# Optimization experiments

Hardware: AMD Instinct MI355X
Metric: run time of the kernel (lower is better)

Reference implementation:

```python
import jax, jax.numpy as jnp
import numpy as np

B, T, D, F = 32, 512, 512, 256
K = 3
MEL_MAX = 4096
EPS = 1e-5


def _xavier(key, shape, fan_in, fan_out):
    lim = float(np.sqrt(6.0 / (fan_in + fan_out)))
    return jax.random.uniform(key, shape, jnp.float32, -lim, lim)


def setup_inputs() -> dict:
    key = jax.random.key(0)
    ks = jax.random.split(key, 6)
    x = jax.random.normal(ks[0], (B, T, D), jnp.float32)
    target = jax.random.randint(ks[1], (B, T), 0, 8)  # per-token durations
    # conv weights stored as [K, I, O] (lax 'WIO'); torch xavier on [O,I,K]: fan_in=I*K, fan_out=O*K
    w1 = _xavier(ks[2], (K, D, F), D * K, F * K)
    b1 = jnp.zeros((F,), jnp.float32)
    g1 = jnp.ones((F,), jnp.float32)
    be1 = jnp.zeros((F,), jnp.float32)
    w2 = _xavier(ks[3], (K, F, F), F * K, F * K)
    b2 = jnp.zeros((F,), jnp.float32)
    g2 = jnp.ones((F,), jnp.float32)
    be2 = jnp.zeros((F,), jnp.float32)
    wl = _xavier(ks[4], (F, 1), F, 1)
    bl = jnp.zeros((1,), jnp.float32)
    return dict(x=x, target=target, mel_max_length=MEL_MAX,
                w1=w1, b1=b1, g1=g1, be1=be1,
                w2=w2, b2=b2, g2=g2, be2=be2, wl=wl, bl=bl)


def _layer_norm(h, g, b):
    mu = jnp.mean(h, axis=-1, keepdims=True)
    var = jnp.mean(jnp.square(h - mu), axis=-1, keepdims=True)
    return (h - mu) * jax.lax.rsqrt(var + EPS) * g + b


def _conv1d(h, w, b):
    # h: [B,T,C_in], w: [K,C_in,C_out]; torch padding=1 with K=3 == SAME
    out = jax.lax.conv_general_dilated(h, w, (1,), 'SAME',
                                       dimension_numbers=('NWC', 'WIO', 'NWC'))
    return out + b


def reference(x, target, mel_max_length, w1, b1, g1, be1, w2, b2, g2, be2, wl, bl):
    # ---- DurationPredictor (eval: dropout = identity) ----
    h = jax.nn.relu(_layer_norm(_conv1d(x, w1, b1), g1, be1))
    h = jax.nn.relu(_layer_norm(_conv1d(h, w2, b2), g2, be2))
    dur_pred = jax.nn.relu(h @ wl + bl)[..., 0]  # [B, T]

    # ---- LR: ragged expansion of x by `target` durations, padded to mel_max_length ----
    cum = jnp.cumsum(target, axis=1)              # [B, T]
    total = cum[:, -1]                            # [B]
    pos = jnp.arange(mel_max_length)              # [M]
    # frame m maps to token i with cum[i-1] <= m < cum[i]
    idx = jax.vmap(lambda c: jnp.searchsorted(c, pos, side='right'))(cum)  # [B, M]
    idx = jnp.clip(idx, 0, x.shape[1] - 1)
    mask = pos[None, :] < total[:, None]          # [B, M]
    out = jnp.take_along_axis(x, idx[..., None], axis=1) * mask[..., None].astype(x.dtype)
    return (out, dur_pred)
```

## Files before the change

### kernel.cpp

```cpp
#include <hip/hip_runtime.h>
#include <type_traits>

#define B_   32
#define T_   512
#define D_   512
#define F_   256
#define MEL  4096
#define EPS_ 1e-5f

typedef __attribute__((ext_vector_type(8))) short bf16x8;
typedef __attribute__((ext_vector_type(4))) float f32x4;

#define GLL16(gp, lp) \
    __builtin_amdgcn_global_load_lds((const __attribute__((address_space(1))) void*)(gp), \
                                     (__attribute__((address_space(3))) void*)(lp), 16, 0, 0)
#define BARRIER() do { asm volatile("" ::: "memory"); __builtin_amdgcn_s_barrier(); \
                       asm volatile("" ::: "memory"); } while (0)
#define MEMPIN() asm volatile("" ::: "memory")

__device__ inline unsigned short f2bf(float f) {
    unsigned u = __float_as_uint(f);
    unsigned r = (u + 0x7fff + ((u >> 16) & 1)) >> 16;
    return (unsigned short)r;
}

#define PREP_WBLOCKS 2304

__global__ __launch_bounds__(256)
void prep_kernel(const float* __restrict__ w1, const float* __restrict__ w2,
                 const int* __restrict__ tgt,
                 unsigned short* __restrict__ w1T, unsigned short* __restrict__ w2T,
                 int* __restrict__ gidx)
{
    __shared__ int lcum[T_];
    __shared__ int wsum[4];

    int bid = blockIdx.x;
    int tid = threadIdx.x;
    if (bid < PREP_WBLOCKS) {
        int idx = bid * 256 + tid;
        if (idx < 3 * D_ * F_) {
            int kk = idx / F_, f = idx % F_;
            w1T[(size_t)f * (3 * D_) + kk] = f2bf(w1[idx]);
        } else {
            int j = idx - 3 * D_ * F_;
            int kk = j / F_, f = j % F_;
            w2T[(size_t)f * (3 * F_) + kk] = f2bf(w2[j]);
        }
        return;
    }

    int b = bid - PREP_WBLOCKS;
    int t0 = tid * 2;
    int a0 = tgt[b * T_ + t0], a1 = tgt[b * T_ + t0 + 1];
    int lane = tid & 63, w = tid >> 6;
    int v = a0 + a1;
#pragma unroll
    for (int o = 1; o < 64; o <<= 1) { int u = __shfl_up(v, o); if (lane >= o) v += u; }
    if (lane == 63) wsum[w] = v;
    __syncthreads();
    int base = 0;
#pragma unroll
    for (int i = 0; i < 4; ++i) if (i < w) base += wsum[i];
    int incl = base + v;
    lcum[t0]     = incl - a1;
    lcum[t0 + 1] = incl;
    __syncthreads();

    int total = lcum[T_ - 1];
#pragma unroll
    for (int k = 0; k < MEL / 256; ++k) {
        int pos = tid + k * 256;
        int lo = 0, hi = T_;
        while (lo < hi) { int mid = (lo + hi) >> 1; if (lcum[mid] <= pos) lo = mid + 1; else hi = mid; }
        gidx[b * MEL + pos] = (pos < total) ? min(lo, T_ - 1) : -1;
    }
}

template<int IN_D, typename InT, bool FUSE_DUR, int GP, int GBASE>
__global__ __launch_bounds__(512)
void conv_mfma_kernel(const InT* __restrict__ x, const unsigned short* __restrict__ wT,
                      const float* __restrict__ bias, const float* __restrict__ gamma,
                      const float* __restrict__ beta, unsigned short* __restrict__ out,
                      const float* __restrict__ wl, const float* __restrict__ bl,
                      float* __restrict__ dur,
                      const float* __restrict__ xf, const int* __restrict__ gidx,
                      float* __restrict__ gout)
{
    constexpr int MT = 64;
    constexpr int KT = 3 * IN_D;
    constexpr int PHASES = KT / 64;

    __shared__ __align__(16) char xs_raw[(MT + 2) * IN_D * 2];
    __shared__ __align__(16) unsigned short xsB[2 * 16384];
    __shared__ float red[MT][8];
    __shared__ float redD[MT][4];

    const int blocksPerBatch = T_ / MT;
    const int b  = blockIdx.x / blocksPerBatch;
    const int t0 = (blockIdx.x % blocksPerBatch) * MT;
    const int l  = threadIdx.x & 63;
    const int wv = threadIdx.x >> 6;
    const int fg = wv & 3;
    const int rg = wv >> 2;

    constexpr int CH = (MT + 2) * IN_D / 8;
    for (int c = threadIdx.x; c < CH; c += 512) {
        int j  = c / (IN_D / 8);
        int d8 = (c % (IN_D / 8)) * 8;
        int t  = t0 - 1 + j;
        uint4 pk = make_uint4(0u, 0u, 0u, 0u);
        if (t >= 0 && t < T_) {
            if constexpr (std::is_same_v<InT, float>) {
                const float4* src = reinterpret_cast<const float4*>(&x[((size_t)b * T_ + t) * IN_D + d8]);
                float4 a0 = src[0], a1 = src[1];
                pk.x = (unsigned)f2bf(a0.x) | ((unsigned)f2bf(a0.y) << 16);
                pk.y = (unsigned)f2bf(a0.z) | ((unsigned)f2bf(a0.w) << 16);
                pk.z = (unsigned)f2bf(a1.x) | ((unsigned)f2bf(a1.y) << 16);
                pk.w = (unsigned)f2bf(a1.z) | ((unsigned)f2bf(a1.w) << 16);
            } else {
                pk = *reinterpret_cast<const uint4*>(&x[((size_t)b * T_ + t) * IN_D + d8]);
            }
        }
        int byte = ((j * IN_D + d8) * 2) ^ ((j & 7) << 4);
        *reinterpret_cast<uint4*>(&xs_raw[byte]) = pk;
    }

    float bv[4], gv[4], bev[4], wlv[4];
#pragma unroll
    for (int n = 0; n < 4; ++n) {
        int f = fg * 64 + n * 16 + (l & 15);
        bv[n] = bias[f]; gv[n] = gamma[f]; bev[n] = beta[f];
        if constexpr (FUSE_DUR) wlv[n] = wl[f];
    }
    float blv = 0.f;
    if constexpr (FUSE_DUR) blv = bl[0];

    asm volatile("s_waitcnt vmcnt(0)" ::: "memory");
    __syncthreads();

    constexpr int GROWS = 2 * GP;
    const int rbase = GBASE + (blockIdx.x * 8 + wv) * GROWS;
    int gidxv = gidx[rbase + min(l, GROWS - 1)];
    MEMPIN();

    const int sbase = wv * 4;
    auto stageB = [&](int ph, int buf) {
        int p = ph < PHASES ? ph : PHASES - 1;
        unsigned short* lb = &xsB[buf * 16384];
#pragma unroll
        for (int i = 0; i < 4; ++i) {
            int s = sbase + i;
            int c = s * 64 + l;
            int f = c >> 3;
            int kg = (c & 7) ^ (f & 7);
            const unsigned short* src = wT + (size_t)f * KT + p * 64 + kg * 8;
            GLL16(src, lb + s * 512);
        }
    };
    auto loadBfrag = [&](bf16x8* dst, int buf, int kk2) {
#pragma unroll
        for (int n = 0; n < 4; ++n) {
            int f  = fg * 64 + n * 16 + (l & 15);
            int kg = kk2 * 4 + (l >> 4);
            dst[n] = *reinterpret_cast<const bf16x8*>(&xsB[buf * 16384 + f * 64 + ((kg ^ (f & 7)) * 8)]);
        }
    };
    const int k_lane = (l >> 4) * 8;
    auto loadA = [&](bf16x8* dst, int kk) {
        int kp = kk / IN_D;
        int dbase = (kk % IN_D) + k_lane;
#pragma unroll
        for (int m = 0; m < 2; ++m) {
            int j = rg * 32 + m * 16 + (l & 15) + kp;
            int byte = ((j * IN_D + dbase) * 2) ^ ((j & 7) << 4);
            dst[m] = *reinterpret_cast<const bf16x8*>(&xs_raw[byte]);
        }
    };

    float4 ga[3][2][2];
    auto loadSet = [&](int slot, int s) {
#pragma unroll
        for (int i = 0; i < 2; ++i) {
            int li = 2 * s + i;
            int ix = __shfl(gidxv, li);
            int r  = rbase + li;
            const float* src = xf + ((size_t)(r >> 12) * T_ + max(ix, 0)) * D_ + l * 4;
            ga[slot][i][0] = *reinterpret_cast<const float4*>(src);
            ga[slot][i][1] = *reinterpret_cast<const float4*>(src + 256);
        }
    };
    auto storeSet = [&](int slot, int s) {
#pragma unroll
        for (int i = 0; i < 2; ++i) {
            int li = 2 * s + i;
            int ix = __shfl(gidxv, li);
            int r  = rbase + li;
            float4 a = ga[slot][i][0], c = ga[slot][i][1];
            if (ix < 0) { a = make_float4(0.f,0.f,0.f,0.f); c = make_float4(0.f,0.f,0.f,0.f); }
            float* d = gout + (size_t)r * D_ + l * 4;
            *reinterpret_cast<float4*>(d)       = a;
            *reinterpret_cast<float4*>(d + 256) = c;
        }
    };

    f32x4 acc[2][4];
#pragma unroll
    for (int m = 0; m < 2; ++m)
#pragma unroll
        for (int n = 0; n < 4; ++n) acc[m][n] = (f32x4){0.f, 0.f, 0.f, 0.f};

    stageB(0, 0);  MEMPIN();
    stageB(1, 1);  MEMPIN();
    loadSet(0, 0); MEMPIN();
    loadSet(1, 1); MEMPIN();

#pragma unroll
    for (int p = 0; p < PHASES; ++p) {
        const int nw = (p == 0) ? 12 : (p == 1) ? 16
                     : 4 * (1 + ((p >= 3 && p - 3 < GP) ? 1 : 0) + ((p < GP) ? 1 : 0) +
                                ((p - 2 < GP) ? 1 : 0) + ((p + 1 < GP) ? 1 : 0));
        if      (nw == 20) asm volatile("s_waitcnt vmcnt(20)" ::: "memory");
        else if (nw == 16) asm volatile("s_waitcnt vmcnt(16)" ::: "memory");
        else if (nw == 12) asm volatile("s_waitcnt vmcnt(12)" ::: "memory");
        else if (nw == 8)  asm volatile("s_waitcnt vmcnt(8)"  ::: "memory");
        else               asm volatile("s_waitcnt vmcnt(4)"  ::: "memory");
        BARRIER();
        int buf = p & 1;
#pragma unroll
        for (int kk2 = 0; kk2 < 2; ++kk2) {
            int kk = p * 64 + kk2 * 32;
            bf16x8 Bv[4], Av[2];
            loadBfrag(Bv, buf, kk2);
            loadA(Av, kk);
#pragma unroll
            for (int m = 0; m < 2; ++m)
#pragma unroll
                for (int n = 0; n < 4; ++n)
                    acc[m][n] = __builtin_amdgcn_mfma_f32_16x16x32_bf16(Av[m], Bv[n], acc[m][n], 0, 0, 0);
        }
        BARRIER();
        stageB(p + 2, buf);                                  MEMPIN();
        if (p >= 1 && p - 1 < GP) { storeSet((p - 1) % 3, p - 1); MEMPIN(); }
        if (p + 2 < GP)           { loadSet((p + 2) % 3, p + 2); MEMPIN(); }
    }
    if constexpr (GP >= PHASES) {
        storeSet((GP - 1) % 3, GP - 1);
    }

#pragma unroll
    for (int m = 0; m < 2; ++m)
#pragma unroll
        for (int q = 0; q < 4; ++q) {
            float s = 0.f, s2 = 0.f;
#pragma unroll
            for (int n = 0; n < 4; ++n) {
                float v2 = acc[m][n][q] + bv[n];
                acc[m][n][q] = v2;
                s += v2; s2 += v2 * v2;
            }
#pragma unroll
            for (int o = 1; o < 16; o <<= 1) { s += __shfl_xor(s, o); s2 += __shfl_xor(s2, o); }
            int row = rg * 32 + m * 16 + (l >> 4) * 4 + q;
            if ((l & 15) == 0) { red[row][fg * 2] = s; red[row][fg * 2 + 1] = s2; }
        }
    __syncthreads();

#pragma unroll
    for (int m = 0; m < 2; ++m)
#pragma unroll
        for (int q = 0; q < 4; ++q) {
            int row = rg * 32 + m * 16 + (l >> 4) * 4 + q;
            float s  = red[row][0] + red[row][2] + red[row][4] + red[row][6];
            float s2 = red[row][1] + red[row][3] + red[row][5] + red[row][7];
            float mu  = s * (1.f / F_);
            float var = s2 * (1.f / F_) - mu * mu;
            float rs  = rsqrtf(var + EPS_);
            size_t rb2 = ((size_t)(b * T_ + t0 + row)) * F_;
            float part = 0.f;
#pragma unroll
            for (int n = 0; n < 4; ++n) {
                float y = (acc[m][n][q] - mu) * rs * gv[n] + bev[n];
                y = fmaxf(y, 0.f);
                out[rb2 + fg * 64 + n * 16 + (l & 15)] = f2bf(y);
                if constexpr (FUSE_DUR) part = fmaf(y, wlv[n], part);
            }
            if constexpr (FUSE_DUR) {
#pragma unroll
                for (int o = 1; o < 16; o <<= 1) part += __shfl_xor(part, o);
                if ((l & 15) == 0) redD[row][fg] = part;
            }
        }

    if constexpr (FUSE_DUR) {
        __syncthreads();
        if (threadIdx.x < MT) {
            float s = redD[threadIdx.x][0] + redD[threadIdx.x][1]
                    + redD[threadIdx.x][2] + redD[threadIdx.x][3] + blv;
            dur[(size_t)b * T_ + t0 + threadIdx.x] = fmaxf(s, 0.f);
        }
    }
}

extern "C" void kernel_launch(void* const* d_in, const int* in_sizes, int n_in,
                              void* d_out, int out_size, void* d_ws, size_t ws_size,
                              hipStream_t stream)
{
    const float* x      = (const float*)d_in[0];
    const int*   target = (const int*)d_in[1];
    const float* w1  = (const float*)d_in[3];
    const float* b1  = (const float*)d_in[4];
    const float* g1  = (const float*)d_in[5];
    const float* be1 = (const float*)d_in[6];
    const float* w2  = (const float*)d_in[7];
    const float* b2  = (const float*)d_in[8];
    const float* g2  = (const float*)d_in[9];
    const float* be2 = (const float*)d_in[10];
    const float* wl  = (const float*)d_in[11];
    const float* bl  = (const float*)d_in[12];

    float* out = (float*)d_out;
    float* dur = out + (size_t)B_ * MEL * D_;

    char* ws = (char*)d_ws;
    unsigned short* w1T = (unsigned short*)ws;         ws += (size_t)F_ * (3 * D_) * 2;
    unsigned short* w2T = (unsigned short*)ws;         ws += (size_t)F_ * (3 * F_) * 2;
    unsigned short* h1  = (unsigned short*)ws;         ws += (size_t)B_ * T_ * F_ * 2;
    unsigned short* h2  = (unsigned short*)ws;         ws += (size_t)B_ * T_ * F_ * 2;
    int*            gidx = (int*)ws;

    prep_kernel<<<PREP_WBLOCKS + B_, 256, 0, stream>>>(w1, w2, target, w1T, w2T, gidx);

    conv_mfma_kernel<D_, float, false, 24, 0><<<B_ * (T_ / 64), 512, 0, stream>>>(
        x, w1T, b1, g1, be1, h1, nullptr, nullptr, nullptr, x, gidx, out);
    conv_mfma_kernel<F_, unsigned short, true, 8, 98304><<<B_ * (T_ / 64), 512, 0, stream>>>(
        h1, w2T, b2, g2, be2, h2, wl, bl, dur, x, gidx, out);
}
```

Measured before the change: 97.43 us.

## Load conv weight fragments directly from global into registers, drop LDS staging

Replaces the double-buffered LDS staging of weight tiles (global_load_lds plus barriers and hand-tuned vmcnt waits) with per-lane direct global loads of B fragments into a three-deep register ring, removing the per-phase block barriers. The interleaved gather load/store schedule is re-timed to the new 32-wide k-steps, and launch bounds request two blocks per CU since the LDS footprint shrinks. In exchange it adds register pressure, gives up LDS reuse of weights across waves (each wave fetches its own slices from L2), and issues uncoalesced strided global reads.

```diff
diff --git a/kernel.cpp b/kernel.cpp
--- a/kernel.cpp
+++ b/kernel.cpp
@@ -11,11 +11,6 @@
 typedef __attribute__((ext_vector_type(8))) short bf16x8;
 typedef __attribute__((ext_vector_type(4))) float f32x4;
 
-#define GLL16(gp, lp) \
-    __builtin_amdgcn_global_load_lds((const __attribute__((address_space(1))) void*)(gp), \
-                                     (__attribute__((address_space(3))) void*)(lp), 16, 0, 0)
-#define BARRIER() do { asm volatile("" ::: "memory"); __builtin_amdgcn_s_barrier(); \
-                       asm volatile("" ::: "memory"); } while (0)
 #define MEMPIN() asm volatile("" ::: "memory")
 
 __device__ inline unsigned short f2bf(float f) {
@@ -78,7 +73,7 @@
 }
 
 template<int IN_D, typename InT, bool FUSE_DUR, int GP, int GBASE>
-__global__ __launch_bounds__(512)
+__global__ __launch_bounds__(512, 2)
 void conv_mfma_kernel(const InT* __restrict__ x, const unsigned short* __restrict__ wT,
                       const float* __restrict__ bias, const float* __restrict__ gamma,
                       const float* __restrict__ beta, unsigned short* __restrict__ out,
@@ -89,10 +84,10 @@
 {
     constexpr int MT = 64;
     constexpr int KT = 3 * IN_D;
-    constexpr int PHASES = KT / 64;
+    constexpr int KSTEPS = KT / 32;
+    static_assert(2 * GP <= KSTEPS, "gather sets must fit in even steps");
 
     __shared__ __align__(16) char xs_raw[(MT + 2) * IN_D * 2];
-    __shared__ __align__(16) unsigned short xsB[2 * 16384];
     __shared__ float red[MT][8];
     __shared__ float redD[MT][4];
 
@@ -136,7 +131,6 @@
     float blv = 0.f;
     if constexpr (FUSE_DUR) blv = bl[0];
 
-    asm volatile("s_waitcnt vmcnt(0)" ::: "memory");
     __syncthreads();
 
     constexpr int GROWS = 2 * GP;
@@ -144,29 +138,16 @@
     int gidxv = gidx[rbase + min(l, GROWS - 1)];
     MEMPIN();
 
-    const int sbase = wv * 4;
-    auto stageB = [&](int ph, int buf) {
-        int p = ph < PHASES ? ph : PHASES - 1;
-        unsigned short* lb = &xsB[buf * 16384];
-#pragma unroll
-        for (int i = 0; i < 4; ++i) {
-            int s = sbase + i;
-            int c = s * 64 + l;
-            int f = c >> 3;
-            int kg = (c & 7) ^ (f & 7);
-            const unsigned short* src = wT + (size_t)f * KT + p * 64 + kg * 8;
-            GLL16(src, lb + s * 512);
+    const int f_lane = fg * 64 + (l & 15);
+    const int k_lane = (l >> 4) * 8;
+    auto loadB = [&](bf16x8* dst, int s) {
+        if (s < KSTEPS) {
+            const unsigned short* p = &wT[(size_t)f_lane * KT + s * 32 + k_lane];
+#pragma unroll
+            for (int n = 0; n < 4; ++n)
+                dst[n] = *reinterpret_cast<const bf16x8*>(p + (size_t)n * 16 * KT);
         }
     };
-    auto loadBfrag = [&](bf16x8* dst, int buf, int kk2) {
-#pragma unroll
-        for (int n = 0; n < 4; ++n) {
-            int f  = fg * 64 + n * 16 + (l & 15);
-            int kg = kk2 * 4 + (l >> 4);
-            dst[n] = *reinterpret_cast<const bf16x8*>(&xsB[buf * 16384 + f * 64 + ((kg ^ (f & 7)) * 8)]);
-        }
-    };
-    const int k_lane = (l >> 4) * 8;
     auto loadA = [&](bf16x8* dst, int kk) {
         int kp = kk / IN_D;
         int dbase = (kk % IN_D) + k_lane;
@@ -210,43 +191,35 @@
 #pragma unroll
         for (int n = 0; n < 4; ++n) acc[m][n] = (f32x4){0.f, 0.f, 0.f, 0.f};
 
-    stageB(0, 0);  MEMPIN();
-    stageB(1, 1);  MEMPIN();
-    loadSet(0, 0); MEMPIN();
-    loadSet(1, 1); MEMPIN();
-
-#pragma unroll
-    for (int p = 0; p < PHASES; ++p) {
-        const int nw = (p == 0) ? 12 : (p == 1) ? 16
-                     : 4 * (1 + ((p >= 3 && p - 3 < GP) ? 1 : 0) + ((p < GP) ? 1 : 0) +
-                                ((p - 2 < GP) ? 1 : 0) + ((p + 1 < GP) ? 1 : 0));
-        if      (nw == 20) asm volatile("s_waitcnt vmcnt(20)" ::: "memory");
-        else if (nw == 16) asm volatile("s_waitcnt vmcnt(16)" ::: "memory");
-        else if (nw == 12) asm volatile("s_waitcnt vmcnt(12)" ::: "memory");
-        else if (nw == 8)  asm volatile("s_waitcnt vmcnt(8)"  ::: "memory");
-        else               asm volatile("s_waitcnt vmcnt(4)"  ::: "memory");
-        BARRIER();
-        int buf = p & 1;
-#pragma unroll
-        for (int kk2 = 0; kk2 < 2; ++kk2) {
-            int kk = p * 64 + kk2 * 32;
-            bf16x8 Bv[4], Av[2];
-            loadBfrag(Bv, buf, kk2);
-            loadA(Av, kk);
+    bf16x8 Bq[3][4];
+    loadB(Bq[0], 0); MEMPIN();
+    loadB(Bq[1], 1); MEMPIN();
+    loadB(Bq[2], 2); MEMPIN();
+
+#pragma unroll
+    for (int s = 0; s < KSTEPS; ++s) {
+        bf16x8 Av[2];
+        loadA(Av, s * 32);
+        {
+            bf16x8* Bv = Bq[s % 3];
 #pragma unroll
             for (int m = 0; m < 2; ++m)
 #pragma unroll
                 for (int n = 0; n < 4; ++n)
                     acc[m][n] = __builtin_amdgcn_mfma_f32_16x16x32_bf16(Av[m], Bv[n], acc[m][n], 0, 0, 0);
         }
-        BARRIER();
-        stageB(p + 2, buf);                                  MEMPIN();
-        if (p >= 1 && p - 1 < GP) { storeSet((p - 1) % 3, p - 1); MEMPIN(); }
-        if (p + 2 < GP)           { loadSet((p + 2) % 3, p + 2); MEMPIN(); }
-    }
-    if constexpr (GP >= PHASES) {
-        storeSet((GP - 1) % 3, GP - 1);
-    }
+        MEMPIN();
+        loadB(Bq[s % 3], s + 3);
+        MEMPIN();
+        if ((s & 1) == 0) {
+            int q = s >> 1;
+            if (q >= 3 && q - 3 < GP) { storeSet((q - 3) % 3, q - 3); MEMPIN(); }
+            if (q < GP)               { loadSet(q % 3, q);            MEMPIN(); }
+        }
+    }
+#pragma unroll
+    for (int j = (KSTEPS / 2 >= 3 ? KSTEPS / 2 - 3 : 0); j < GP; ++j)
+        storeSet(j % 3, j);
 
 #pragma unroll
     for (int m = 0; m < 2; ++m)
```

Result: slower. 129.0 us (+32.4%).

## Fuse both conv layers into one kernel with halo recompute in LDS

Applied to the files above, without the earlier changes.

Merges the two conv+LayerNorm kernels into a single kernel. Each block computes conv1 for 66 rows (its 64 plus a one-row halo on each side), writes the activated result as bf16 into shared memory, then runs conv2 from LDS. This removes the h1/h2 global round trips and one launch. The gather of 64 output rows per wave is now spread over one kernel instead of two. The cost is redundant halo MFMA work done by a subset of waves, a larger LDS footprint that may limit occupancy, and the h2 global write is dropped since it was unused.

```diff
diff --git a/kernel.cpp b/kernel.cpp
--- a/kernel.cpp
+++ b/kernel.cpp
@@ -1,5 +1,4 @@
 #include <hip/hip_runtime.h>
-#include <type_traits>
 
 #define B_   32
 #define T_   512
@@ -7,6 +6,11 @@
 #define F_   256
 #define MEL  4096
 #define EPS_ 1e-5f
+
+#define PH1  24
+#define PH2  12
+#define PHT  36
+#define GP   32
 
 typedef __attribute__((ext_vector_type(8))) short bf16x8;
 typedef __attribute__((ext_vector_type(4))) float f32x4;
@@ -77,84 +81,75 @@
     }
 }
 
-template<int IN_D, typename InT, bool FUSE_DUR, int GP, int GBASE>
 __global__ __launch_bounds__(512)
-void conv_mfma_kernel(const InT* __restrict__ x, const unsigned short* __restrict__ wT,
-                      const float* __restrict__ bias, const float* __restrict__ gamma,
-                      const float* __restrict__ beta, unsigned short* __restrict__ out,
-                      const float* __restrict__ wl, const float* __restrict__ bl,
-                      float* __restrict__ dur,
-                      const float* __restrict__ xf, const int* __restrict__ gidx,
-                      float* __restrict__ gout)
+void fused_kernel(const float* __restrict__ x,
+                  const unsigned short* __restrict__ w1T, const unsigned short* __restrict__ w2T,
+                  const float* __restrict__ b1, const float* __restrict__ g1, const float* __restrict__ be1,
+                  const float* __restrict__ b2, const float* __restrict__ g2, const float* __restrict__ be2,
+                  const float* __restrict__ wl, const float* __restrict__ bl,
+                  const int* __restrict__ gidx,
+                  float* __restrict__ out, float* __restrict__ dur)
 {
-    constexpr int MT = 64;
-    constexpr int KT = 3 * IN_D;
-    constexpr int PHASES = KT / 64;
-
-    __shared__ __align__(16) char xs_raw[(MT + 2) * IN_D * 2];
+    __shared__ __align__(16) char xsA[84 * 512 * 2];
     __shared__ __align__(16) unsigned short xsB[2 * 16384];
-    __shared__ float red[MT][8];
-    __shared__ float redD[MT][4];
-
-    const int blocksPerBatch = T_ / MT;
-    const int b  = blockIdx.x / blocksPerBatch;
-    const int t0 = (blockIdx.x % blocksPerBatch) * MT;
+    __shared__ float red[80][8];
+    __shared__ float redD[64][4];
+
+    const int b  = blockIdx.x >> 3;
+    const int t0 = (blockIdx.x & 7) * 64;
     const int l  = threadIdx.x & 63;
     const int wv = threadIdx.x >> 6;
     const int fg = wv & 3;
     const int rg = wv >> 2;
 
-    constexpr int CH = (MT + 2) * IN_D / 8;
-    for (int c = threadIdx.x; c < CH; c += 512) {
-        int j  = c / (IN_D / 8);
-        int d8 = (c % (IN_D / 8)) * 8;
-        int t  = t0 - 1 + j;
+    for (int c = threadIdx.x; c < 68 * 64; c += 512) {
+        int j  = c >> 6;
+        int d8 = (c & 63) * 8;
+        int t  = t0 - 2 + j;
         uint4 pk = make_uint4(0u, 0u, 0u, 0u);
         if (t >= 0 && t < T_) {
-            if constexpr (std::is_same_v<InT, float>) {
-                const float4* src = reinterpret_cast<const float4*>(&x[((size_t)b * T_ + t) * IN_D + d8]);
-                float4 a0 = src[0], a1 = src[1];
-                pk.x = (unsigned)f2bf(a0.x) | ((unsigned)f2bf(a0.y) << 16);
-                pk.y = (unsigned)f2bf(a0.z) | ((unsigned)f2bf(a0.w) << 16);
-                pk.z = (unsigned)f2bf(a1.x) | ((unsigned)f2bf(a1.y) << 16);
-                pk.w = (unsigned)f2bf(a1.z) | ((unsigned)f2bf(a1.w) << 16);
-            } else {
-                pk = *reinterpret_cast<const uint4*>(&x[((size_t)b * T_ + t) * IN_D + d8]);
-            }
-        }
-        int byte = ((j * IN_D + d8) * 2) ^ ((j & 7) << 4);
-        *reinterpret_cast<uint4*>(&xs_raw[byte]) = pk;
-    }
-
-    float bv[4], gv[4], bev[4], wlv[4];
+            const float4* src = reinterpret_cast<const float4*>(&x[((size_t)b * T_ + t) * D_ + d8]);
+            float4 a0 = src[0], a1 = src[1];
+            pk.x = (unsigned)f2bf(a0.x) | ((unsigned)f2bf(a0.y) << 16);
+            pk.y = (unsigned)f2bf(a0.z) | ((unsigned)f2bf(a0.w) << 16);
+            pk.z = (unsigned)f2bf(a1.x) | ((unsigned)f2bf(a1.y) << 16);
+            pk.w = (unsigned)f2bf(a1.z) | ((unsigned)f2bf(a1.w) << 16);
+        }
+        int byte = ((j * 512 + d8) * 2) ^ ((j & 7) << 4);
+        *reinterpret_cast<uint4*>(&xsA[byte]) = pk;
+    }
+
+    float bv1[4], gv1[4], bev1[4], bv2[4], gv2[4], bev2[4], wlv[4];
 #pragma unroll
     for (int n = 0; n < 4; ++n) {
         int f = fg * 64 + n * 16 + (l & 15);
-        bv[n] = bias[f]; gv[n] = gamma[f]; bev[n] = beta[f];
-        if constexpr (FUSE_DUR) wlv[n] = wl[f];
-    }
-    float blv = 0.f;
-    if constexpr (FUSE_DUR) blv = bl[0];
+        bv1[n] = b1[f]; gv1[n] = g1[f]; bev1[n] = be1[f];
+        bv2[n] = b2[f]; gv2[n] = g2[f]; bev2[n] = be2[f];
+        wlv[n] = wl[f];
+    }
+    float blv = bl[0];
 
     asm volatile("s_waitcnt vmcnt(0)" ::: "memory");
     __syncthreads();
 
-    constexpr int GROWS = 2 * GP;
-    const int rbase = GBASE + (blockIdx.x * 8 + wv) * GROWS;
-    int gidxv = gidx[rbase + min(l, GROWS - 1)];
+    const int rbase = (blockIdx.x * 8 + wv) * 64;
+    int gidxv = gidx[rbase + l];
     MEMPIN();
 
     const int sbase = wv * 4;
     auto stageB = [&](int ph, int buf) {
-        int p = ph < PHASES ? ph : PHASES - 1;
         unsigned short* lb = &xsB[buf * 16384];
+        const unsigned short* wsrc;
+        int KTc, phc;
+        if (ph < PH1) { wsrc = w1T; KTc = 1536; phc = ph; }
+        else          { wsrc = w2T; KTc = 768;  phc = (ph - PH1 < PH2) ? ph - PH1 : PH2 - 1; }
 #pragma unroll
         for (int i = 0; i < 4; ++i) {
             int s = sbase + i;
             int c = s * 64 + l;
             int f = c >> 3;
             int kg = (c & 7) ^ (f & 7);
-            const unsigned short* src = wT + (size_t)f * KT + p * 64 + kg * 8;
+            const unsigned short* src = wsrc + (size_t)f * KTc + phc * 64 + kg * 8;
             GLL16(src, lb + s * 512);
         }
     };
@@ -167,16 +162,6 @@
         }
     };
     const int k_lane = (l >> 4) * 8;
-    auto loadA = [&](bf16x8* dst, int kk) {
-        int kp = kk / IN_D;
-        int dbase = (kk % IN_D) + k_lane;
-#pragma unroll
-        for (int m = 0; m < 2; ++m) {
-            int j = rg * 32 + m * 16 + (l & 15) + kp;
-            int byte = ((j * IN_D + dbase) * 2) ^ ((j & 7) << 4);
-            dst[m] = *reinterpret_cast<const bf16x8*>(&xs_raw[byte]);
-        }
-    };
 
     float4 ga[3][2][2];
     auto loadSet = [&](int slot, int s) {
@@ -185,7 +170,7 @@
             int li = 2 * s + i;
             int ix = __shfl(gidxv, li);
             int r  = rbase + li;
-            const float* src = xf + ((size_t)(r >> 12) * T_ + max(ix, 0)) * D_ + l * 4;
+            const float* src = x + ((size_t)(r >> 12) * T_ + max(ix, 0)) * D_ + l * 4;
             ga[slot][i][0] = *reinterpret_cast<const float4*>(src);
             ga[slot][i][1] = *reinterpret_cast<const float4*>(src + 256);
         }
@@ -198,17 +183,20 @@
             int r  = rbase + li;
             float4 a = ga[slot][i][0], c = ga[slot][i][1];
             if (ix < 0) { a = make_float4(0.f,0.f,0.f,0.f); c = make_float4(0.f,0.f,0.f,0.f); }
-            float* d = gout + (size_t)r * D_ + l * 4;
+            float* d = out + (size_t)r * D_ + l * 4;
             *reinterpret_cast<float4*>(d)       = a;
             *reinterpret_cast<float4*>(d + 256) = c;
         }
     };
 
-    f32x4 acc[2][4];
-#pragma unroll
-    for (int m = 0; m < 2; ++m)
-#pragma unroll
-        for (int n = 0; n < 4; ++n) acc[m][n] = (f32x4){0.f, 0.f, 0.f, 0.f};
+    f32x4 acc1[3][4], acc2[2][4];
+#pragma unroll
+    for (int n = 0; n < 4; ++n) {
+#pragma unroll
+        for (int m = 0; m < 3; ++m) acc1[m][n] = (f32x4){0.f, 0.f, 0.f, 0.f};
+#pragma unroll
+        for (int m = 0; m < 2; ++m) acc2[m][n] = (f32x4){0.f, 0.f, 0.f, 0.f};
+    }
 
     stageB(0, 0);  MEMPIN();
     stageB(1, 1);  MEMPIN();
@@ -216,36 +204,114 @@
     loadSet(1, 1); MEMPIN();
 
 #pragma unroll
-    for (int p = 0; p < PHASES; ++p) {
+    for (int p = 0; p < PHT; ++p) {
         const int nw = (p == 0) ? 12 : (p == 1) ? 16
-                     : 4 * (1 + ((p >= 3 && p - 3 < GP) ? 1 : 0) + ((p < GP) ? 1 : 0) +
-                                ((p - 2 < GP) ? 1 : 0) + ((p + 1 < GP) ? 1 : 0));
+                     : 4 * (1 + ((p >= 3 && p - 3 < GP) ? 1 : 0)
+                              + ((p >= 2 && p < GP) ? 1 : 0)
+                              + ((p - 2 < GP) ? 1 : 0)
+                              + ((p + 1 >= 2 && p + 1 < GP) ? 1 : 0));
         if      (nw == 20) asm volatile("s_waitcnt vmcnt(20)" ::: "memory");
         else if (nw == 16) asm volatile("s_waitcnt vmcnt(16)" ::: "memory");
         else if (nw == 12) asm volatile("s_waitcnt vmcnt(12)" ::: "memory");
         else if (nw == 8)  asm volatile("s_waitcnt vmcnt(8)"  ::: "memory");
         else               asm volatile("s_waitcnt vmcnt(4)"  ::: "memory");
         BARRIER();
-        int buf = p & 1;
+        const int buf = p & 1;
 #pragma unroll
         for (int kk2 = 0; kk2 < 2; ++kk2) {
-            int kk = p * 64 + kk2 * 32;
-            bf16x8 Bv[4], Av[2];
+            bf16x8 Bv[4];
             loadBfrag(Bv, buf, kk2);
-            loadA(Av, kk);
-#pragma unroll
-            for (int m = 0; m < 2; ++m)
-#pragma unroll
-                for (int n = 0; n < 4; ++n)
-                    acc[m][n] = __builtin_amdgcn_mfma_f32_16x16x32_bf16(Av[m], Bv[n], acc[m][n], 0, 0, 0);
+            if (p < PH1) {
+                int kk = p * 64 + kk2 * 32;
+                int kp = kk / 512;
+                int dbase = (kk % 512) + k_lane;
+#pragma unroll
+                for (int m = 0; m < 2; ++m) {
+                    int j = rg * 32 + m * 16 + (l & 15) + kp;
+                    bf16x8 Av = *reinterpret_cast<const bf16x8*>(
+                        &xsA[((j * 512 + dbase) * 2) ^ ((j & 7) << 4)]);
+#pragma unroll
+                    for (int n = 0; n < 4; ++n)
+                        acc1[m][n] = __builtin_amdgcn_mfma_f32_16x16x32_bf16(Av, Bv[n], acc1[m][n], 0, 0, 0);
+                }
+                if (rg == 0) {
+                    int j = 64 + (l & 15) + kp;
+                    bf16x8 Av = *reinterpret_cast<const bf16x8*>(
+                        &xsA[((j * 512 + dbase) * 2) ^ ((j & 7) << 4)]);
+#pragma unroll
+                    for (int n = 0; n < 4; ++n)
+                        acc1[2][n] = __builtin_amdgcn_mfma_f32_16x16x32_bf16(Av, Bv[n], acc1[2][n], 0, 0, 0);
+                }
+            } else {
+                int kk = (p - PH1) * 64 + kk2 * 32;
+                int kp = kk / 256;
+                int dbase = (kk % 256) + k_lane;
+#pragma unroll
+                for (int m = 0; m < 2; ++m) {
+                    int j = rg * 32 + m * 16 + (l & 15) + kp;
+                    bf16x8 Av = *reinterpret_cast<const bf16x8*>(
+                        &xsA[((j * 256 + dbase) * 2) ^ ((j & 7) << 4)]);
+#pragma unroll
+                    for (int n = 0; n < 4; ++n)
+                        acc2[m][n] = __builtin_amdgcn_mfma_f32_16x16x32_bf16(Av, Bv[n], acc2[m][n], 0, 0, 0);
+                }
+            }
         }
         BARRIER();
-        stageB(p + 2, buf);                                  MEMPIN();
+        stageB(p + 2, buf);                                   MEMPIN();
         if (p >= 1 && p - 1 < GP) { storeSet((p - 1) % 3, p - 1); MEMPIN(); }
         if (p + 2 < GP)           { loadSet((p + 2) % 3, p + 2); MEMPIN(); }
-    }
-    if constexpr (GP >= PHASES) {
-        storeSet((GP - 1) % 3, GP - 1);
+
+        if (p == PH1 - 1) {
+            __syncthreads();
+#pragma unroll
+            for (int m = 0; m < 3; ++m) {
+                if (m < 2 || rg == 0) {
+#pragma unroll
+                    for (int q = 0; q < 4; ++q) {
+                        float s = 0.f, s2 = 0.f;
+#pragma unroll
+                        for (int n = 0; n < 4; ++n) {
+                            float v2 = acc1[m][n][q] + bv1[n];
+                            acc1[m][n][q] = v2;
+                            s += v2; s2 += v2 * v2;
+                        }
+#pragma unroll
+                        for (int o = 1; o < 16; o <<= 1) { s += __shfl_xor(s, o); s2 += __shfl_xor(s2, o); }
+                        int row = (m < 2 ? rg * 32 + m * 16 : 64) + (l >> 4) * 4 + q;
+                        if ((l & 15) == 0) { red[row][fg * 2] = s; red[row][fg * 2 + 1] = s2; }
+                    }
+                }
+            }
+            __syncthreads();
+#pragma unroll
+            for (int m = 0; m < 3; ++m) {
+                if (m < 2 || rg == 0) {
+#pragma unroll
+                    for (int q = 0; q < 4; ++q) {
+                        int row = (m < 2 ? rg * 32 + m * 16 : 64) + (l >> 4) * 4 + q;
+                        if (row < 66) {
+                            float s  = red[row][0] + red[row][2] + red[row][4] + red[row][6];
+                            float s2 = red[row][1] + red[row][3] + red[row][5] + red[row][7];
+                            float mu  = s * (1.f / F_);
+                            float var = s2 * (1.f / F_) - mu * mu;
+                            float rs  = rsqrtf(var + EPS_);
+                            int t = t0 - 1 + row;
+                            bool valid = (t >= 0 && t < T_);
+#pragma unroll
+                            for (int n = 0; n < 4; ++n) {
+                                float y = (acc1[m][n][q] - mu) * rs * gv1[n] + bev1[n];
+                                y = fmaxf(y, 0.f);
+                                int col = fg * 64 + n * 16 + (l & 15);
+                                int byte = ((row * 256 + col) * 2) ^ ((row & 7) << 4);
+                                *reinterpret_cast<unsigned short*>(&xsA[byte]) = valid ? f2bf(y) : 0;
+                            }
+                        }
+                    }
+                }
+            }
+            __syncthreads();
+        }
     }
 
 #pragma unroll
@@ -255,8 +321,8 @@
             float s = 0.f, s2 = 0.f;
 #pragma unroll
             for (int n = 0; n < 4; ++n) {
-                float v2 = acc[m][n][q] + bv[n];
-                acc[m][n][q] = v2;
+                float v2 = acc2[m][n][q] + bv2[n];
+                acc2[m][n][q] = v2;
                 s += v2; s2 += v2 * v2;
             }
 #pragma unroll
@@ -276,29 +342,22 @@
             float mu  = s * (1.f / F_);
             float var = s2 * (1.f / F_) - mu * mu;
             float rs  = rsqrtf(var + EPS_);
-            size_t rb2 = ((size_t)(b * T_ + t0 + row)) * F_;
             float part = 0.f;
 #pragma unroll
             for (int n = 0; n < 4; ++n) {
-                float y = (acc[m][n][q] - mu) * rs * gv[n] + bev[n];
-                y = fmaxf(y, 0.f);
-                out[rb2 + fg * 64 + n * 16 + (l & 15)] = f2bf(y);
-                if constexpr (FUSE_DUR) part = fmaf(y, wlv[n], part);
-            }
-            if constexpr (FUSE_DUR) {
-#pragma unroll
-                for (int o = 1; o < 16; o <<= 1) part += __shfl_xor(part, o);
-                if ((l & 15) == 0) redD[row][fg] = part;
-            }
-        }
-
-    if constexpr (FUSE_DUR) {
-        __syncthreads();
-        if (threadIdx.x < MT) {
-            float s = redD[threadIdx.x][0] + redD[threadIdx.x][1]
-                    + redD[threadIdx.x][2] + redD[threadIdx.x][3] + blv;
-            dur[(size_t)b * T_ + t0 + threadIdx.x] = fmaxf(s, 0.f);
-        }
+                float y = (acc2[m][n][q] - mu) * rs * gv2[n] + bev2[n];
+                part = fmaf(fmaxf(y, 0.f), wlv[n], part);
+            }
+#pragma unroll
+            for (int o = 1; o < 16; o <<= 1) part += __shfl_xor(part, o);
+            if ((l & 15) == 0) redD[row][fg] = part;
+        }
+    __syncthreads();
+
+    if (threadIdx.x < 64) {
+        float s = redD[threadIdx.x][0] + redD[threadIdx.x][1]
+                + redD[threadIdx.x][2] + redD[threadIdx.x][3] + blv;
+        dur[(size_t)b * T_ + t0 + threadIdx.x] = fmaxf(s, 0.f);
     }
 }
 
@@ -325,14 +384,10 @@
     char* ws = (char*)d_ws;
     unsigned short* w1T = (unsigned short*)ws;         ws += (size_t)F_ * (3 * D_) * 2;
     unsigned short* w2T = (unsigned short*)ws;         ws += (size_t)F_ * (3 * F_) * 2;
-    unsigned short* h1  = (unsigned short*)ws;         ws += (size_t)B_ * T_ * F_ * 2;
-    unsigned short* h2  = (unsigned short*)ws;         ws += (size_t)B_ * T_ * F_ * 2;
     int*            gidx = (int*)ws;
 
     prep_kernel<<<PREP_WBLOCKS + B_, 256, 0, stream>>>(w1, w2, target, w1T, w2T, gidx);
 
-    conv_mfma_kernel<D_, float, false, 24, 0><<<B_ * (T_ / 64), 512, 0, stream>>>(
-        x, w1T, b1, g1, be1, h1, nullptr, nullptr, nullptr, x, gidx, out);
-    conv_mfma_kernel<F_, unsigned short, true, 8, 98304><<<B_ * (T_ / 64), 512, 0, stream>>>(
-        h1, w2T, b2, g2, be2, h2, wl, bl, dur, x, gidx, out);
+    fused_kernel<<<B_ * (T_ / 64), 512, 0, stream>>>(
+        x, w1T, w2T, b1, g1, be1, b2, g2, be2, wl, bl, gidx, out, dur);
 }
```

Result: slower. 168.3 us (+72.7%).
